# Optimization experiments

Hardware: AMD Instinct MI355X
Metric: run time of the kernel (lower is better)

## Reference

```python
import jax, jax.numpy as jnp
import numpy as np

B, CIN, COUT, H, W = 4, 64, 64, 192, 192
KS, N, EPS = 3, 9, 1e-5


def setup_inputs() -> dict:
    key = jax.random.key(0)
    ks = jax.random.split(key, 4)
    return {
        "inputs": jax.random.normal(ks[0], (B, CIN, H, W), jnp.float32),
        "w_p": jax.random.normal(ks[1], (2 * N, CIN, KS, KS), jnp.float32) * 0.01,
        "b_p": jnp.zeros((2 * N,), jnp.float32),
        "w_m": jax.random.normal(ks[2], (N, CIN, KS, KS), jnp.float32) * 0.05,
        "b_m": jnp.zeros((N,), jnp.float32),
        "w_conv": jax.random.normal(ks[3], (COUT, CIN, KS, KS), jnp.float32) * (1.0 / np.sqrt(CIN * N)),
        "gamma": jnp.ones((COUT,), jnp.float32),
        "beta": jnp.zeros((COUT,), jnp.float32),
    }


def _conv3x3(x, w, b):
    y = jax.lax.conv_general_dilated(x, w, (1, 1), ((1, 1), (1, 1)),
                                     dimension_numbers=("NCHW", "OIHW", "NCHW"))
    return y + b[None, :, None, None]


def reference(inputs, w_p, b_p, w_m, b_m, w_conv, gamma, beta):
    x = inputs
    b, c, h, w = x.shape
    offset = _conv3x3(x, w_p, b_p)                 # (B, 2N, H, W)
    m = jax.nn.sigmoid(_conv3x3(x, w_m, b_m))      # (B, N, H, W)

    xp = jnp.pad(x, ((0, 0), (0, 0), (1, 1), (1, 1)))  # zero pad by 1
    hp, wp = h + 2, w + 2

    off = offset.transpose(0, 2, 3, 1)             # (B, H, W, 2N), first N=y, last N=x
    ky, kx = jnp.meshgrid(jnp.arange(-1, 2), jnp.arange(-1, 2), indexing="ij")
    pny = ky.reshape(-1).astype(x.dtype)           # (N,) kernel dy, ky-major order
    pnx = kx.reshape(-1).astype(x.dtype)
    p0y = jnp.arange(1, h + 1, dtype=x.dtype)      # base coords in padded image
    p0x = jnp.arange(1, w + 1, dtype=x.dtype)

    py = p0y[None, :, None, None] + pny + off[..., :N]   # (B, H, W, N)
    px = p0x[None, None, :, None] + pnx + off[..., N:]

    qy0 = jnp.clip(jnp.floor(py), 0, hp - 1)
    qy1 = jnp.clip(jnp.floor(py) + 1, 0, hp - 1)
    qx0 = jnp.clip(jnp.floor(px), 0, wp - 1)
    qx1 = jnp.clip(jnp.floor(px) + 1, 0, wp - 1)
    pyc = jnp.clip(py, 0, hp - 1)
    pxc = jnp.clip(px, 0, wp - 1)

    g_lt = (1 + (qy0 - pyc)) * (1 + (qx0 - pxc))
    g_rb = (1 - (qy1 - pyc)) * (1 - (qx1 - pxc))
    g_lb = (1 + (qy0 - pyc)) * (1 - (qx1 - pxc))
    g_rt = (1 - (qy1 - pyc)) * (1 + (qx0 - pxc))

    xf = xp.reshape(b, c, hp * wp)

    def gather(qy, qx):
        idx = (qy.astype(jnp.int32) * wp + qx.astype(jnp.int32)).reshape(b, 1, -1)
        idx = jnp.broadcast_to(idx, (b, c, idx.shape[-1]))
        return jnp.take_along_axis(xf, idx, axis=2).reshape(b, c, h, w, N)

    x_s = (g_lt[:, None] * gather(qy0, qx0)
           + g_rb[:, None] * gather(qy1, qx1)
           + g_lb[:, None] * gather(qy0, qx1)
           + g_rt[:, None] * gather(qy1, qx0))          # (B, C, H, W, N)
    x_s = x_s * m.transpose(0, 2, 3, 1)[:, None]        # modulation (B,1,H,W,N)

    # main conv over the 9 sampled taps (== conv with stride=ks on rearranged tensor)
    out = jnp.einsum("bchwn,ocn->bohw", x_s, w_conv.reshape(w_conv.shape[0], c, N))

    # BatchNorm2d (training mode: batch stats), ReLU, MaxPool(2)
    mu = out.mean((0, 2, 3), keepdims=True)
    var = ((out - mu) ** 2).mean((0, 2, 3), keepdims=True)
    out = gamma[None, :, None, None] * (out - mu) * jax.lax.rsqrt(var + EPS) + beta[None, :, None, None]
    out = jax.nn.relu(out)
    bo, co, ho, wo = out.shape
    out = out.reshape(bo, co, ho // 2, 2, wo // 2, 2).max(axis=(3, 5))
    return out
```

## Files before the change

kernel.cpp:

```cpp
#include <hip/hip_runtime.h>
#include <hip/hip_bf16.h>
#include <math.h>

#define HW     192
#define PLANE  (HW*HW)
#define CIN    64
#define COUT   64
#define NB     4
#define NPIX   (NB*PLANE)
#define H2     194
#define W2     200
#define WR     7
#define WC     21
#define NPOS   (WR*WC)

typedef __attribute__((ext_vector_type(8))) short bf16x8;
typedef __attribute__((ext_vector_type(4))) float f32x4;
typedef __attribute__((ext_vector_type(2))) float f32x2;

static __device__ __forceinline__ ushort f2bf(float f) {
    __hip_bfloat16 h = __float2bfloat16(f);
    return __builtin_bit_cast(ushort, h);
}
static __device__ __forceinline__ float bf2f(ushort u) {
    return __builtin_bit_cast(float, ((unsigned)u) << 16);
}
static __device__ __forceinline__ f32x2 up2(unsigned u) {
    f32x2 r;
    r.x = __builtin_bit_cast(float, u << 16);
    r.y = __builtin_bit_cast(float, u & 0xffff0000u);
    return r;
}

__global__ __launch_bounds__(256) void kpadprep(
    const float* __restrict__ x,
    const float* __restrict__ wc, const float* __restrict__ w_p,
    const float* __restrict__ w_m,
    ushort* __restrict__ xt, ushort* __restrict__ wbf, ushort* __restrict__ womf)
{
    int blk = blockIdx.x;
    int t   = threadIdx.x;
    if (blk < NB * H2) {
        __shared__ ushort sT[W2 * 72];
        int b = blk / H2, y = blk % H2;
        bool yok = (y >= 1 && y <= HW);
        const float* xb = x + (size_t)b * CIN * PLANE + (size_t)(y - 1) * HW;
        {
            int zi  = t >> 5;
            int col = (zi == 0) ? 0 : 192 + zi;
            *(unsigned*)&sT[col * 72 + (t & 31) * 2] = 0;
        }
#pragma unroll
        for (int it = 0; it < 6; ++it) {
            int idx = t + 256 * it;
            int cp  = idx / 48;
            int q   = idx - cp * 48;
            int c   = cp * 2;
            float4 v0 = make_float4(0.f, 0.f, 0.f, 0.f), v1 = v0;
            if (yok) {
                v0 = *(const float4*)(xb + (size_t)c * PLANE + 4 * q);
                v1 = *(const float4*)(xb + (size_t)(c + 1) * PLANE + 4 * q);
            }
            float a0[4] = {v0.x, v0.y, v0.z, v0.w};
            float a1[4] = {v1.x, v1.y, v1.z, v1.w};
#pragma unroll
            for (int j = 0; j < 4; ++j)
                *(unsigned*)&sT[(4 * q + 1 + j) * 72 + c] =
                    (unsigned)f2bf(a0[j]) | ((unsigned)f2bf(a1[j]) << 16);
        }
        __syncthreads();
        uint4* dst = (uint4*)(xt + ((size_t)(b * H2 + y) * W2) * 64);
#pragma unroll
        for (int it = 0; it < 7; ++it) {
            int idx = t + 256 * it;
            if (idx < 1600) {
                int col = idx >> 3, g = idx & 7;
                dst[col * 8 + g] = *(uint4*)&sT[col * 72 + g * 8];
            }
        }
        return;
    }
    int i = (blk - NB * H2) * 256 + t;
    if (i < 4608) {
        int lane  = i & 63;
        int rc    = i >> 6;
        int chunk = rc % 18;
        int og    = rc / 18;
        int o  = og * 16 + (lane & 15);
        int k0 = chunk * 32 + (lane >> 4) * 8;
        ushort v[8];
#pragma unroll
        for (int j = 0; j < 8; ++j) {
            int k = k0 + j, c = k & 63, n = k >> 6;
            v[j] = f2bf(wc[o * 576 + c * 9 + n]);
        }
        ((uint4*)wbf)[i] = *(uint4*)v;
    } else if (i < 6912) {
        int ii    = i - 4608;
        int lane  = ii & 63;
        int rc    = ii >> 6;
        int chunk = rc % 18;
        int og    = rc / 18;
        int co = og * 16 + (lane & 15);
        int k0 = chunk * 32 + (lane >> 4) * 8;
        ushort v[8];
#pragma unroll
        for (int j = 0; j < 8; ++j) {
            int k = k0 + j, c = k & 63, n = k >> 6;
            float w = 0.f;
            if (co < 18)      w = w_p[(co * 64 + c) * 9 + n];
            else if (co < 27) w = w_m[((co - 18) * 64 + c) * 9 + n];
            v[j] = f2bf(w);
        }
        ((uint4*)womf)[ii] = *(uint4*)v;
    }
}

__global__ __launch_bounds__(256, 4) void kdeform(
    const ushort* __restrict__ xt,
    const ushort* __restrict__ wbf, const ushort* __restrict__ womf,
    const float* __restrict__ b_p, const float* __restrict__ b_m,
    ushort* __restrict__ outp)
{
    __shared__ __align__(16) char smem[40708];
    ushort* sWin = (ushort*)smem;
    ushort* sXF  = (ushort*)(smem + 18816);
    float (*sOMa)[17] = (float(*)[17])(smem + 18816);
    float (*sOMb)[17] = (float(*)[17])(smem + 18816 + 2176);
    float4 (*sG)[16] = (float4(*)[16])(smem + 37248);
    uint (*sPos)[16] = (uint(*)[16])(smem + 39552);
    uint (*sOg)[16]  = (uint(*)[16])(smem + 40128);
    int* sFlag = (int*)(smem + 40704);

    int t    = threadIdx.x;
    int pix0 = blockIdx.x * 16;
    int b    = pix0 / PLANE;
    int rem  = pix0 - b * PLANE;
    int h    = rem / HW;
    int w0   = rem - h * HW;
    int rbase = min(max(h - 2, 0), H2 - WR);
    int wbase = min(max(w0 - 2, 0), W2 - WC - 4);
    if (t == 0) *sFlag = 0;

    const ushort* xtb = xt + (size_t)(b * H2) * W2 * 64;

    {
        const uint4* gsrc = (const uint4*)(xtb + ((size_t)rbase * W2 + wbase) * 64);
#pragma unroll
        for (int it = 0; it < 5; ++it) {
            int idx = t + 256 * it;
            if (idx < NPOS * 8) {
                int pos = idx >> 3, s = idx & 7;
                int g   = (s - pos) & 7;
                int r   = (pos * 3121) >> 16;
                int cc  = pos - r * WC;
                *(uint4*)&sWin[pos * 64 + s * 8] = gsrc[((r * W2 + cc) << 3) + g];
            }
        }
    }
    __syncthreads();

    {
        int lane = t & 63;
        int wv   = t >> 6;
        int og   = wv & 1;
        int half = wv >> 1;
        int sub  = lane >> 4;
        int hr   = h - rbase;
        int wrp  = w0 - wbase + (lane & 15);
        f32x4 acc = {0.f, 0.f, 0.f, 0.f};
#pragma unroll
        for (int cc = 0; cc < 9; ++cc) {
            int chunk = half * 9 + cc;
            bf16x8 a = *(const bf16x8*)&womf[((og * 18 + chunk) * 64 + lane) * 8];
            int n  = chunk >> 1;
            int dy = n / 3, dx = n - dy * 3;
            int pos  = (hr + dy) * WC + wrp + dx;
            int slot = ((chunk & 1) * 4 + sub + pos) & 7;
            bf16x8 bb = *(const bf16x8*)&sWin[pos * 64 + slot * 8];
            acc = __builtin_amdgcn_mfma_f32_16x16x32_bf16(a, bb, acc, 0, 0, 0);
        }
        int col = lane & 15, row0 = sub * 4;
        float (*dst)[17] = half ? sOMb : sOMa;
#pragma unroll
        for (int r = 0; r < 4; ++r) dst[og * 16 + row0 + r][col] = acc[r];
    }
    __syncthreads();

    uint pkC = 0, ogC = 0; float4 gC = make_float4(0.f, 0.f, 0.f, 0.f);
    if (t < 144) {
        int pp = t & 15, n = t >> 4;
        float offy = sOMa[n][pp]      + sOMb[n][pp]      + b_p[n];
        float offx = sOMa[9 + n][pp]  + sOMb[9 + n][pp]  + b_p[9 + n];
        float mr   = sOMa[18 + n][pp] + sOMb[18 + n][pp] + b_m[n];
        float m = 1.f / (1.f + __expf(-mr));
        int dy = n / 3, dx = n - dy * 3;
        float py = (float)(h + dy) + offy;
        float px = (float)(w0 + pp + dx) + offx;
        float fy = floorf(py), fx = floorf(px);
        float qy0 = fminf(fmaxf(fy,       0.f), 193.f);
        float qy1 = fminf(fmaxf(fy + 1.f, 0.f), 193.f);
        float qx0 = fminf(fmaxf(fx,       0.f), 193.f);
        float qx1 = fminf(fmaxf(fx + 1.f, 0.f), 193.f);
        float pyc = fminf(fmaxf(py, 0.f), 193.f);
        float pxc = fminf(fmaxf(px, 0.f), 193.f);
        float ay = 1.f + qy0 - pyc, by = 1.f - (qy1 - pyc);
        float ax = 1.f + qx0 - pxc, bx = 1.f - (qx1 - pxc);
        int ry0 = (int)qy0, ry1 = (int)qy1;
        int cx0 = (int)qx0, cx1 = (int)qx1;
        int xs  = cx1 - cx0;
        ogC = (uint)(ry0 | (ry1 << 8) | (cx0 << 16) | (xs << 24));
        int p00 = (ry0 - rbase) * WC + (cx0 - wbase);
        int p10 = (ry1 - rbase) * WC + (cx0 - wbase);
        pkC = (uint)((p00 & 255) | (((p00 + xs) & 255) << 8)
                   | ((p10 & 255) << 16) | (((p10 + xs) & 255) << 24));
        gC = make_float4(ay * ax * m, ay * bx * m, by * ax * m, by * bx * m);
        if (ry0 < rbase || ry1 > rbase + (WR - 1) ||
            cx0 < wbase || cx1 > wbase + (WC - 1))
            atomicOr(sFlag, 1);
    }
    __syncthreads();
    if (t < 144) {
        int pp = t & 15, n = t >> 4;
        sOg[n][pp]  = ogC;
        sPos[n][pp] = pkC;
        sG[n][pp]   = gC;
    }
    __syncthreads();

    {
        int px  = t & 15, sub = t >> 4;
        int o8  = sub & 7;
        bool fb = (*sFlag != 0);
#pragma unroll
        for (int it = 0; it < 5; ++it) {
            int item = sub + 16 * it;
            if (item >= 72) break;
            int n = item >> 3;
            float4 G = sG[n][px];
            uint4 A0, A1, C0, C1;
            if (!fb) {
                uint pk = sPos[n][px];
                int p00 = pk & 255, p01 = (pk >> 8) & 255;
                int p10 = (pk >> 16) & 255, p11 = pk >> 24;
                A0 = *(const uint4*)&sWin[p00 * 64 + ((o8 + p00) & 7) * 8];
                A1 = *(const uint4*)&sWin[p01 * 64 + ((o8 + p01) & 7) * 8];
                C0 = *(const uint4*)&sWin[p10 * 64 + ((o8 + p10) & 7) * 8];
                C1 = *(const uint4*)&sWin[p11 * 64 + ((o8 + p11) & 7) * 8];
            } else {
                uint gp = sOg[n][px];
                int ry0 = gp & 255, ry1 = (gp >> 8) & 255;
                int cx0 = (gp >> 16) & 255, xs = gp >> 24;
                const ushort* g0 = xtb + (size_t)(ry0 * W2 + cx0) * 64 + o8 * 8;
                const ushort* g1 = xtb + (size_t)(ry1 * W2 + cx0) * 64 + o8 * 8;
                A0 = *(const uint4*)g0;
                A1 = *(const uint4*)(g0 + xs * 64);
                C0 = *(const uint4*)g1;
                C1 = *(const uint4*)(g1 + xs * 64);
            }
            unsigned ua0[4] = {A0.x, A0.y, A0.z, A0.w};
            unsigned ua1[4] = {A1.x, A1.y, A1.z, A1.w};
            unsigned uc0[4] = {C0.x, C0.y, C0.z, C0.w};
            unsigned uc1[4] = {C1.x, C1.y, C1.z, C1.w};
            ushort pk8[8] __attribute__((aligned(16)));
#pragma unroll
            for (int q = 0; q < 4; ++q) {
                f32x2 v = G.x * up2(ua0[q]) + G.y * up2(ua1[q])
                        + G.z * up2(uc0[q]) + G.w * up2(uc1[q]);
                pk8[2 * q]     = f2bf(v.x);
                pk8[2 * q + 1] = f2bf(v.y);
            }
            int chunk = n * 2 + (o8 >> 2), s16 = o8 & 3;
            *(uint4*)&sXF[(chunk * 64 + s16 * 16 + (px ^ s16)) * 8] = *(uint4*)pk8;
        }
    }
    __syncthreads();

    {
        int lane = t & 63, og = t >> 6;
        int sub = lane >> 4, pcol = lane & 15;
        f32x4 acc = {0.f, 0.f, 0.f, 0.f};
#pragma unroll
        for (int chunk = 0; chunk < 18; ++chunk) {
            bf16x8 a  = *(const bf16x8*)&wbf[((og * 18 + chunk) * 64 + lane) * 8];
            bf16x8 bb = *(const bf16x8*)&sXF[(chunk * 64 + sub * 16 + (pcol ^ sub)) * 8];
            acc = __builtin_amdgcn_mfma_f32_16x16x32_bf16(a, bb, acc, 0, 0, 0);
        }
        int row0 = sub * 4;
        ushort* ob = outp + ((size_t)(b * COUT + og * 16 + row0)) * PLANE + rem + pcol;
        ob[0]                 = f2bf(acc[0]);
        ob[(size_t)PLANE]     = f2bf(acc[1]);
        ob[2 * (size_t)PLANE] = f2bf(acc[2]);
        ob[3 * (size_t)PLANE] = f2bf(acc[3]);
    }
}

__global__ __launch_bounds__(256) void kstats(
    const ushort* __restrict__ outp, float* __restrict__ partial)
{
    int o  = blockIdx.x >> 3;
    int sl = blockIdx.x & 7;
    int t  = threadIdx.x;
    float s = 0.f, s2 = 0.f;
    for (int b = 0; b < NB; ++b) {
        const uint4* pl = (const uint4*)(outp + ((size_t)(b * COUT + o)) * PLANE
                                         + sl * (PLANE / 8));
        for (int i = t; i < PLANE / 64; i += 256) {
            uint4 v = pl[i];
            unsigned ua[4] = {v.x, v.y, v.z, v.w};
#pragma unroll
            for (int j = 0; j < 4; ++j) {
                float lo = __builtin_bit_cast(float, ua[j] << 16);
                float hi = __builtin_bit_cast(float, ua[j] & 0xffff0000u);
                s  += lo + hi;
                s2 += lo * lo + hi * hi;
            }
        }
    }
    __shared__ float rs[256], rs2[256];
    rs[t] = s; rs2[t] = s2;
    __syncthreads();
    for (int st = 128; st > 0; st >>= 1) {
        if (t < st) { rs[t] += rs[t + st]; rs2[t] += rs2[t + st]; }
        __syncthreads();
    }
    if (t == 0) {
        partial[o * 8 + sl]       = rs[0];
        partial[512 + o * 8 + sl] = rs2[0];
    }
}

__global__ __launch_bounds__(256) void kbnpool(
    const ushort* __restrict__ outp, const float* __restrict__ partial,
    const float* __restrict__ gamma, const float* __restrict__ beta,
    float* __restrict__ out)
{
    int i = blockIdx.x * 256 + threadIdx.x;
    int wo  = i % 96;
    int tmp = i / 96;
    int ho  = tmp % 96; tmp /= 96;
    int o   = tmp % 64;
    int b   = tmp / 64;
    float s = 0.f, s2 = 0.f;
#pragma unroll
    for (int sl = 0; sl < 8; ++sl) {
        s  += partial[o * 8 + sl];
        s2 += partial[512 + o * 8 + sl];
    }
    float inv  = 1.f / (float)(NB * PLANE);
    float mean = s * inv;
    float var  = s2 * inv - mean * mean;
    float rsq  = rsqrtf(var + 1e-5f);
    float g  = gamma[o] * rsq;
    float bt = beta[o] - mean * g;
    const ushort* pl = outp + ((size_t)(b * COUT + o)) * PLANE + (2 * ho) * HW + 2 * wo;
    unsigned u01 = *(const unsigned*)pl;
    unsigned u23 = *(const unsigned*)(pl + HW);
    float y00 = fmaxf(g * bf2f((ushort)(u01 & 0xffff)) + bt, 0.f);
    float y01 = fmaxf(g * bf2f((ushort)(u01 >> 16))    + bt, 0.f);
    float y10 = fmaxf(g * bf2f((ushort)(u23 & 0xffff)) + bt, 0.f);
    float y11 = fmaxf(g * bf2f((ushort)(u23 >> 16))    + bt, 0.f);
    out[i] = fmaxf(fmaxf(y00, y01), fmaxf(y10, y11));
}

extern "C" void kernel_launch(void* const* d_in, const int* in_sizes, int n_in,
                              void* d_out, int out_size, void* d_ws, size_t ws_size,
                              hipStream_t stream)
{
    const float* x      = (const float*)d_in[0];
    const float* w_p    = (const float*)d_in[1];
    const float* b_p    = (const float*)d_in[2];
    const float* w_m    = (const float*)d_in[3];
    const float* b_m    = (const float*)d_in[4];
    const float* w_conv = (const float*)d_in[5];
    const float* gamma  = (const float*)d_in[6];
    const float* beta   = (const float*)d_in[7];
    float* out = (float*)d_out;

    char* ws = (char*)d_ws;
    ushort* xt      = (ushort*)ws;
    ushort* outp    = (ushort*)(ws + 19865600);
    float*  partial = (float*)(ws + 38739968);
    ushort* wbf     = (ushort*)(ws + 38744064);
    ushort* womf    = (ushort*)(ws + 38817792);

    kpadprep<<<NB * H2 + 27, 256, 0, stream>>>(x, w_conv, w_p, w_m, xt, wbf, womf);
    kdeform<<<NPIX / 16, 256, 0, stream>>>(xt, wbf, womf, b_p, b_m, outp);
    kstats<<<512, 256, 0, stream>>>(outp, partial);
    kbnpool<<<(NB * COUT * 96 * 96) / 256, 256, 0, stream>>>(outp, partial, gamma, beta, out);
}
```

Before: 180.3 us.

## Fuse BN statistics into deform kernel epilogue and add small finalize kernel

```diff
diff --git a/kernel.cpp b/kernel.cpp
--- a/kernel.cpp
+++ b/kernel.cpp
@@ -8,6 +8,7 @@
 #define COUT   64
 #define NB     4
 #define NPIX   (NB*PLANE)
+#define NBLK   (NPIX/16)
 #define H2     194
 #define W2     200
 #define WR     7
@@ -29,6 +30,12 @@
     f32x2 r;
     r.x = __builtin_bit_cast(float, u << 16);
     r.y = __builtin_bit_cast(float, u & 0xffff0000u);
+    return r;
+}
+static __device__ __forceinline__ unsigned pkbf(float a, float b) {
+    __hip_bfloat162 b2 = __float22bfloat162_rn(make_float2(a, b));
+    unsigned r;
+    __builtin_memcpy(&r, &b2, sizeof(r));
     return r;
 }
 
@@ -120,7 +127,8 @@
     const ushort* __restrict__ xt,
     const ushort* __restrict__ wbf, const ushort* __restrict__ womf,
     const float* __restrict__ b_p, const float* __restrict__ b_m,
-    ushort* __restrict__ outp)
+    ushort* __restrict__ outp,
+    float* __restrict__ partial)
 {
     __shared__ __align__(16) char smem[40708];
     ushort* sWin = (ushort*)smem;
@@ -262,16 +270,15 @@
             unsigned ua1[4] = {A1.x, A1.y, A1.z, A1.w};
             unsigned uc0[4] = {C0.x, C0.y, C0.z, C0.w};
             unsigned uc1[4] = {C1.x, C1.y, C1.z, C1.w};
-            ushort pk8[8] __attribute__((aligned(16)));
+            unsigned pk4[4] __attribute__((aligned(16)));
 #pragma unroll
             for (int q = 0; q < 4; ++q) {
                 f32x2 v = G.x * up2(ua0[q]) + G.y * up2(ua1[q])
                         + G.z * up2(uc0[q]) + G.w * up2(uc1[q]);
-                pk8[2 * q]     = f2bf(v.x);
-                pk8[2 * q + 1] = f2bf(v.y);
+                pk4[q] = pkbf(v.x, v.y);
             }
             int chunk = n * 2 + (o8 >> 2), s16 = o8 & 3;
-            *(uint4*)&sXF[(chunk * 64 + s16 * 16 + (px ^ s16)) * 8] = *(uint4*)pk8;
+            *(uint4*)&sXF[(chunk * 64 + s16 * 16 + (px ^ s16)) * 8] = *(uint4*)pk4;
         }
     }
     __syncthreads();
@@ -292,30 +299,45 @@
         ob[(size_t)PLANE]     = f2bf(acc[1]);
         ob[2 * (size_t)PLANE] = f2bf(acc[2]);
         ob[3 * (size_t)PLANE] = f2bf(acc[3]);
-    }
-}
-
-__global__ __launch_bounds__(256) void kstats(
-    const ushort* __restrict__ outp, float* __restrict__ partial)
+
+        float s[4], s2[4];
+#pragma unroll
+        for (int r = 0; r < 4; ++r) { s[r] = acc[r]; s2[r] = acc[r] * acc[r]; }
+#pragma unroll
+        for (int m = 1; m < 16; m <<= 1) {
+#pragma unroll
+            for (int r = 0; r < 4; ++r) {
+                s[r]  += __shfl_xor(s[r],  m);
+                s2[r] += __shfl_xor(s2[r], m);
+            }
+        }
+        if (pcol == 0) {
+#pragma unroll
+            for (int r = 0; r < 4; ++r) {
+                int ch = og * 16 + row0 + r;
+                partial[(size_t)ch * NBLK + blockIdx.x]        = s[r];
+                partial[(size_t)(64 + ch) * NBLK + blockIdx.x] = s2[r];
+            }
+        }
+    }
+}
+
+__global__ __launch_bounds__(256) void kfinal(
+    const float* __restrict__ partial,
+    const float* __restrict__ gamma, const float* __restrict__ beta,
+    float* __restrict__ stats)
 {
-    int o  = blockIdx.x >> 3;
-    int sl = blockIdx.x & 7;
-    int t  = threadIdx.x;
+    int o = blockIdx.x;
+    int t = threadIdx.x;
     float s = 0.f, s2 = 0.f;
-    for (int b = 0; b < NB; ++b) {
-        const uint4* pl = (const uint4*)(outp + ((size_t)(b * COUT + o)) * PLANE
-                                         + sl * (PLANE / 8));
-        for (int i = t; i < PLANE / 64; i += 256) {
-            uint4 v = pl[i];
-            unsigned ua[4] = {v.x, v.y, v.z, v.w};
-#pragma unroll
-            for (int j = 0; j < 4; ++j) {
-                float lo = __builtin_bit_cast(float, ua[j] << 16);
-                float hi = __builtin_bit_cast(float, ua[j] & 0xffff0000u);
-                s  += lo + hi;
-                s2 += lo * lo + hi * hi;
-            }
-        }
+    const float4* p1 = (const float4*)(partial + (size_t)o * NBLK);
+    const float4* p2 = (const float4*)(partial + (size_t)(64 + o) * NBLK);
+#pragma unroll
+    for (int it = 0; it < 9; ++it) {
+        int i = t + 256 * it;
+        float4 v1 = p1[i], v2 = p2[i];
+        s  += v1.x + v1.y + v1.z + v1.w;
+        s2 += v2.x + v2.y + v2.z + v2.w;
     }
     __shared__ float rs[256], rs2[256];
     rs[t] = s; rs2[t] = s2;
@@ -325,13 +347,18 @@
         __syncthreads();
     }
     if (t == 0) {
-        partial[o * 8 + sl]       = rs[0];
-        partial[512 + o * 8 + sl] = rs2[0];
+        float inv  = 1.f / (float)(NB * PLANE);
+        float mean = rs[0] * inv;
+        float var  = rs2[0] * inv - mean * mean;
+        float rsq  = rsqrtf(var + 1e-5f);
+        float g = gamma[o] * rsq;
+        stats[o]      = g;
+        stats[64 + o] = beta[o] - mean * g;
     }
 }
 
 __global__ __launch_bounds__(256) void kbnpool(
-    const ushort* __restrict__ outp, const float* __restrict__ partial,
+    const ushort* __restrict__ outp, const float* __restrict__ stats,
     const float* __restrict__ gamma, const float* __restrict__ beta,
     float* __restrict__ out)
 {
@@ -341,18 +368,8 @@
     int ho  = tmp % 96; tmp /= 96;
     int o   = tmp % 64;
     int b   = tmp / 64;
-    float s = 0.f, s2 = 0.f;
-#pragma unroll
-    for (int sl = 0; sl < 8; ++sl) {
-        s  += partial[o * 8 + sl];
-        s2 += partial[512 + o * 8 + sl];
-    }
-    float inv  = 1.f / (float)(NB * PLANE);
-    float mean = s * inv;
-    float var  = s2 * inv - mean * mean;
-    float rsq  = rsqrtf(var + 1e-5f);
-    float g  = gamma[o] * rsq;
-    float bt = beta[o] - mean * g;
+    float g  = stats[o];
+    float bt = stats[64 + o];
     const ushort* pl = outp + ((size_t)(b * COUT + o)) * PLANE + (2 * ho) * HW + 2 * wo;
     unsigned u01 = *(const unsigned*)pl;
     unsigned u23 = *(const unsigned*)(pl + HW);
@@ -381,11 +398,12 @@
     ushort* xt      = (ushort*)ws;
     ushort* outp    = (ushort*)(ws + 19865600);
     float*  partial = (float*)(ws + 38739968);
-    ushort* wbf     = (ushort*)(ws + 38744064);
-    ushort* womf    = (ushort*)(ws + 38817792);
+    float*  stats   = (float*)(ws + 43458560);
+    ushort* wbf     = (ushort*)(ws + 43459072);
+    ushort* womf    = (ushort*)(ws + 43532800);
 
     kpadprep<<<NB * H2 + 27, 256, 0, stream>>>(x, w_conv, w_p, w_m, xt, wbf, womf);
-    kdeform<<<NPIX / 16, 256, 0, stream>>>(xt, wbf, womf, b_p, b_m, outp);
-    kstats<<<512, 256, 0, stream>>>(outp, partial);
-    kbnpool<<<(NB * COUT * 96 * 96) / 256, 256, 0, stream>>>(outp, partial, gamma, beta, out);
-}
+    kdeform<<<NBLK, 256, 0, stream>>>(xt, wbf, womf, b_p, b_m, outp, partial);
+    kfinal<<<64, 256, 0, stream>>>(partial, gamma, beta, stats);
+    kbnpool<<<(NB * COUT * 96 * 96) / 256, 256, 0, stream>>>(outp, stats, gamma, beta, out);
+}
```

Measured after the change: 186.4 us. +3.4%, slower.
